# Performance work log

Measured on AMD Instinct MI355X. Metric: run time of the kernel, lower is better.

Reference implementation:

```python
import jax, jax.numpy as jnp
import numpy as np

N_NODES = 110
C = 4096  # in_channels = hidden = out_channels


def setup_inputs() -> dict:
    key = jax.random.key(0)
    ks = jax.random.split(key, 8)
    x = jax.random.normal(ks[0], (N_NODES, C), dtype=jnp.float32)
    adj = jax.random.randint(ks[1], (N_NODES, N_NODES), 0, 2, dtype=jnp.int32)
    # torch.nn.Linear weights stored [out_features, in_features]
    W2 = jax.random.normal(ks[2], (C, C), dtype=jnp.float32) / np.sqrt(C)
    b2 = jax.random.normal(ks[3], (C,), dtype=jnp.float32) * 0.01
    W1 = jax.random.normal(ks[4], (2 * C, C), dtype=jnp.float32) / np.sqrt(2 * C)
    b1 = jax.random.normal(ks[5], (C,), dtype=jnp.float32) * 0.01
    Wl = jax.random.normal(ks[6], (N_NODES, N_NODES), dtype=jnp.float32) / np.sqrt(N_NODES)
    bl = jax.random.normal(ks[7], (N_NODES,), dtype=jnp.float32) * 0.01
    # note: W1 is stored [in=2C, out=C]; W2 [in=C, out=C]; Wl [in=110, out=110]
    return {"x": x, "adj": adj, "W2": W2, "b2": b2, "W1": W1, "b1": b1, "Wl": Wl, "bl": bl}


def reference(x, adj, W2, b2, W1, b1, Wl, bl):
    # FeatGraphConv: h = lin2(x)
    h = x @ W2 + b2  # [N, C]
    # edge_index.nonzero(): adjacency -> edge list (i=src, j=dst); mean-aggregate
    # h[src] at dst. Dense equivalent: column-normalized mask matmul.
    mask = (adj != 0).astype(x.dtype)  # [N, N]
    deg = mask.sum(axis=0)  # in-degree of each target node j
    aggr = (mask.T @ h) / jnp.maximum(deg, 1.0)[:, None]  # [N, C]; 0 for isolated nodes (PyG mean)
    # update: lin1(cat(h, aggr)) then relu (in RegGNN.forward)
    out = jax.nn.relu(jnp.concatenate([h, aggr], axis=1) @ W1 + b1)  # [N, C]
    # x.t(); lin(110,110); x.t()
    out = (out.T @ Wl.T + bl).T  # [N, C]
    return out
```

## Files before the change

### kernel.cpp

```cpp
#include <hip/hip_runtime.h>
#include <hip/hip_fp16.h>

#define C 4096
#define NN 110
#define MPAD 112

typedef _Float16 f16x8 __attribute__((ext_vector_type(8)));
typedef float fx4 __attribute__((ext_vector_type(4)));

__global__ void prep1_kernel(const float* __restrict__ x, _Float16* __restrict__ A1) {
    int idx = blockIdx.x * 256 + threadIdx.x;
    int n = idx >> 12;
    float v = (n < NN) ? x[idx] : 0.f;
    A1[idx] = (_Float16)v;
}

__global__ __launch_bounds__(256, 2)
void mm_kernel(const _Float16* __restrict__ A, const float* __restrict__ B,
               float* __restrict__ Cacc, int lda, int kch) {
    const int t   = threadIdx.x;
    const int wid = blockIdx.x * 4 + (t >> 6);
    const int L   = t & 63;
    const int l15 = L & 15;
    const int q   = L >> 4;
    const int n0  = (wid & 255) * 16;
    const int k0  = (wid >> 8) * kch;

    const _Float16* Ap = A + (size_t)l15 * lda + k0 + q * 8;
    const float*    Bp = B + (size_t)(k0 + q * 8) * C + n0 + l15;

    fx4 acc[7];
    #pragma unroll
    for (int mt = 0; mt < 7; ++mt) acc[mt] = (fx4){0.f, 0.f, 0.f, 0.f};

    float bv0[8], bv1[8];
    f16x8 av0[7], av1[7];

    auto loadB = [&](float (&bv)[8], int kk) {
        #pragma unroll
        for (int j = 0; j < 8; ++j) bv[j] = Bp[(size_t)(kk + j) * C];
    };
    auto loadA = [&](f16x8 (&av)[7], int kk) {
        #pragma unroll
        for (int mt = 0; mt < 7; ++mt)
            av[mt] = *(const f16x8*)(Ap + (size_t)(mt * 16) * lda + kk);
    };
    auto consume = [&](float (&bv)[8], f16x8 (&av)[7]) {
        f16x8 bf;
        #pragma unroll
        for (int j = 0; j < 8; ++j) bf[j] = (_Float16)bv[j];
        #pragma unroll
        for (int mt = 0; mt < 7; ++mt)
            acc[mt] = __builtin_amdgcn_mfma_f32_16x16x32_f16(av[mt], bf, acc[mt], 0, 0, 0);
    };

    loadB(bv0, 0);
    loadA(av0, 0);
    for (int k = 0; k < kch; k += 64) {
        loadB(bv1, k + 32);
        loadA(av1, k + 32);
        consume(bv0, av0);
        if (k + 64 < kch) {
            loadB(bv0, k + 64);
            loadA(av0, k + 64);
        }
        consume(bv1, av1);
    }

    #pragma unroll
    for (int mt = 0; mt < 7; ++mt) {
        #pragma unroll
        for (int r = 0; r < 4; ++r) {
            int row = mt * 16 + q * 4 + r;
            if (row < NN)
                atomicAdd(&Cacc[(size_t)row * C + n0 + l15], acc[mt][r]);
        }
    }
}

__global__ __launch_bounds__(256)
void agg_kernel(const float* __restrict__ h_raw, const int* __restrict__ adj,
                const float* __restrict__ b2, _Float16* __restrict__ A3) {
    __shared__ float hb[NN * 16];
    __shared__ unsigned long long mlo[NN], mhi[NN];
    __shared__ float degs[NN];
    const int t  = threadIdx.x;
    const int c0 = blockIdx.x * 16;

    for (int idx = t; idx < NN * 16; idx += 256) {
        int n = idx >> 4, c = idx & 15;
        float v = h_raw[(size_t)n * C + c0 + c] + b2[c0 + c];
        hb[idx] = v;
        A3[(size_t)n * (2 * C) + c0 + c] = (_Float16)v;
    }
    if (t < 64) {
        int n  = NN + (t >> 5);
        int hs = (t >> 4) & 1;
        int c  = t & 15;
        A3[(size_t)n * (2 * C) + hs * C + c0 + c] = (_Float16)0.f;
    }
    if (t < NN) {
        int j = t;
        unsigned long long lo = 0, hi = 0;
        int dg = 0;
        for (int i = 0; i < 64; ++i) {
            int m = (adj[i * NN + j] != 0);
            lo |= ((unsigned long long)m) << i; dg += m;
        }
        for (int i = 64; i < NN; ++i) {
            int m = (adj[i * NN + j] != 0);
            hi |= ((unsigned long long)m) << (i - 64); dg += m;
        }
        mlo[j] = lo; mhi[j] = hi;
        degs[j] = (float)(dg > 0 ? dg : 1);
    }
    __syncthreads();
    for (int idx = t; idx < NN * 16; idx += 256) {
        int j = idx >> 4, c = idx & 15;
        unsigned long long lo = mlo[j], hi = mhi[j];
        float a = 0.f;
        for (int i = 0; i < 64; ++i)
            if ((lo >> i) & 1) a += hb[i * 16 + c];
        for (int i = 64; i < NN; ++i)
            if ((hi >> (i - 64)) & 1) a += hb[i * 16 + c];
        A3[(size_t)j * (2 * C) + C + c0 + c] = (_Float16)(a / degs[j]);
    }
}

__global__ __launch_bounds__(256)
void fin_kernel(const float* __restrict__ z_raw, const float* __restrict__ b1,
                const float* __restrict__ Wl, const float* __restrict__ bl,
                float* __restrict__ out) {
    __shared__ float zs[NN * 64];
    const int t  = threadIdx.x;
    const int c0 = blockIdx.x * 64;
    const int j  = blockIdx.y * 4 + (t >> 6);
    const int c  = t & 63;

    for (int idx = t; idx < NN * 64; idx += 256) {
        int k = idx >> 6, cc = idx & 63;
        float v = z_raw[(size_t)k * C + c0 + cc] + b1[c0 + cc];
        zs[idx] = fmaxf(v, 0.f);
    }
    __syncthreads();
    if (j < NN) {
        float a = bl[j];
        #pragma unroll 2
        for (int k = 0; k < NN; ++k)
            a += Wl[j * NN + k] * zs[k * 64 + c];
        out[(size_t)j * C + c0 + c] = a;
    }
}

extern "C" void kernel_launch(void* const* d_in, const int* in_sizes, int n_in,
                              void* d_out, int out_size, void* d_ws, size_t ws_size,
                              hipStream_t stream) {
    const float* x   = (const float*)d_in[0];
    const int*   adj = (const int*)d_in[1];
    const float* W2  = (const float*)d_in[2];
    const float* b2  = (const float*)d_in[3];
    const float* W1  = (const float*)d_in[4];
    const float* b1  = (const float*)d_in[5];
    const float* Wl  = (const float*)d_in[6];
    const float* bl  = (const float*)d_in[7];
    float* out = (float*)d_out;

    char* ws = (char*)d_ws;
    float*    h_raw = (float*)(ws);
    float*    z_raw = (float*)(ws + 1802240);
    _Float16* A1    = (_Float16*)(ws + 3604480);
    _Float16* A3    = (_Float16*)(ws + 4521984);

    hipMemsetAsync(d_ws, 0, 3604480, stream);
    prep1_kernel<<<(MPAD * C) / 256, 256, 0, stream>>>(x, A1);
    mm_kernel<<<512, 256, 0, stream>>>(A1, W2, h_raw, C, 512);
    agg_kernel<<<C / 16, 256, 0, stream>>>(h_raw, adj, b2, A3);
    mm_kernel<<<512, 256, 0, stream>>>(A3, W1, z_raw, 2 * C, 1024);
    fin_kernel<<<dim3(C / 64, 28), 256, 0, stream>>>(z_raw, b1, Wl, bl, out);
}
```

Baseline: 391.3 us.

## Stage weight tiles into LDS with async global_load_lds double buffering

```diff
diff --git a/kernel.cpp b/kernel.cpp
--- a/kernel.cpp
+++ b/kernel.cpp
@@ -4,9 +4,15 @@
 #define C 4096
 #define NN 110
 #define MPAD 112
+#define BN 64
+#define BK 128
+#define KCH 512
 
 typedef _Float16 f16x8 __attribute__((ext_vector_type(8)));
 typedef float fx4 __attribute__((ext_vector_type(4)));
+
+#define AS_GLB __attribute__((address_space(1)))
+#define AS_LDS __attribute__((address_space(3)))
 
 __global__ void prep1_kernel(const float* __restrict__ x, _Float16* __restrict__ A1) {
     int idx = blockIdx.x * 256 + threadIdx.x;
@@ -15,56 +21,53 @@
     A1[idx] = (_Float16)v;
 }
 
-__global__ __launch_bounds__(256, 2)
+__global__ __launch_bounds__(256)
 void mm_kernel(const _Float16* __restrict__ A, const float* __restrict__ B,
-               float* __restrict__ Cacc, int lda, int kch) {
+               float* __restrict__ Cacc, int lda) {
+    __shared__ float Bs[2][BK * BN];
     const int t   = threadIdx.x;
-    const int wid = blockIdx.x * 4 + (t >> 6);
+    const int w   = t >> 6;
     const int L   = t & 63;
     const int l15 = L & 15;
     const int q   = L >> 4;
-    const int n0  = (wid & 255) * 16;
-    const int k0  = (wid >> 8) * kch;
+    const int n0  = blockIdx.x * BN;
+    const int k0  = blockIdx.y * KCH;
 
-    const _Float16* Ap = A + (size_t)l15 * lda + k0 + q * 8;
-    const float*    Bp = B + (size_t)(k0 + q * 8) * C + n0 + l15;
+    const float* gsrc = B + (size_t)(k0 + w * 32 + (L >> 4)) * C + n0 + (L & 15) * 4;
+
+    auto stage = [&](int buf, int kc) {
+        #pragma unroll
+        for (int j = 0; j < 8; ++j) {
+            const float* g = gsrc + (size_t)(kc + j * 4) * C;
+            float* l = &Bs[buf][(w * 32 + j * 4) * BN];
+            __builtin_amdgcn_global_load_lds((const AS_GLB void*)g, (AS_LDS void*)l,
+                                             16, 0, 0);
+        }
+    };
 
     fx4 acc[7];
     #pragma unroll
     for (int mt = 0; mt < 7; ++mt) acc[mt] = (fx4){0.f, 0.f, 0.f, 0.f};
 
-    float bv0[8], bv1[8];
-    f16x8 av0[7], av1[7];
-
-    auto loadB = [&](float (&bv)[8], int kk) {
+    stage(0, 0);
+    #pragma unroll 1
+    for (int kc = 0, buf = 0; kc < KCH; kc += BK, buf ^= 1) {
+        __syncthreads();
+        if (kc + BK < KCH) stage(buf ^ 1, kc + BK);
+        const _Float16* Ap = A + (size_t)l15 * lda + k0 + kc + q * 8;
         #pragma unroll
-        for (int j = 0; j < 8; ++j) bv[j] = Bp[(size_t)(kk + j) * C];
-    };
-    auto loadA = [&](f16x8 (&av)[7], int kk) {
-        #pragma unroll
-        for (int mt = 0; mt < 7; ++mt)
-            av[mt] = *(const f16x8*)(Ap + (size_t)(mt * 16) * lda + kk);
-    };
-    auto consume = [&](float (&bv)[8], f16x8 (&av)[7]) {
-        f16x8 bf;
-        #pragma unroll
-        for (int j = 0; j < 8; ++j) bf[j] = (_Float16)bv[j];
-        #pragma unroll
-        for (int mt = 0; mt < 7; ++mt)
-            acc[mt] = __builtin_amdgcn_mfma_f32_16x16x32_f16(av[mt], bf, acc[mt], 0, 0, 0);
-    };
-
-    loadB(bv0, 0);
-    loadA(av0, 0);
-    for (int k = 0; k < kch; k += 64) {
-        loadB(bv1, k + 32);
-        loadA(av1, k + 32);
-        consume(bv0, av0);
-        if (k + 64 < kch) {
-            loadB(bv0, k + 64);
-            loadA(av0, k + 64);
+        for (int s = 0; s < 4; ++s) {
+            f16x8 bfrag;
+            #pragma unroll
+            for (int j = 0; j < 8; ++j)
+                bfrag[j] = (_Float16)Bs[buf][(s * 32 + q * 8 + j) * BN + w * 16 + l15];
+            #pragma unroll
+            for (int mt = 0; mt < 7; ++mt) {
+                f16x8 afrag = *(const f16x8*)(Ap + (size_t)(mt * 16) * lda + s * 32);
+                acc[mt] = __builtin_amdgcn_mfma_f32_16x16x32_f16(afrag, bfrag,
+                                                                 acc[mt], 0, 0, 0);
+            }
         }
-        consume(bv1, av1);
     }
 
     #pragma unroll
@@ -73,7 +76,7 @@
         for (int r = 0; r < 4; ++r) {
             int row = mt * 16 + q * 4 + r;
             if (row < NN)
-                atomicAdd(&Cacc[(size_t)row * C + n0 + l15], acc[mt][r]);
+                atomicAdd(&Cacc[(size_t)row * C + n0 + w * 16 + l15], acc[mt][r]);
         }
     }
 }
@@ -119,10 +122,12 @@
         int j = idx >> 4, c = idx & 15;
         unsigned long long lo = mlo[j], hi = mhi[j];
         float a = 0.f;
+        #pragma unroll 2
         for (int i = 0; i < 64; ++i)
-            if ((lo >> i) & 1) a += hb[i * 16 + c];
+            a = fmaf((float)((lo >> i) & 1ull), hb[i * 16 + c], a);
+        #pragma unroll 2
         for (int i = 64; i < NN; ++i)
-            if ((hi >> (i - 64)) & 1) a += hb[i * 16 + c];
+            a = fmaf((float)((hi >> (i - 64)) & 1ull), hb[i * 16 + c], a);
         A3[(size_t)j * (2 * C) + C + c0 + c] = (_Float16)(a / degs[j]);
     }
 }
@@ -173,8 +178,8 @@
 
     hipMemsetAsync(d_ws, 0, 3604480, stream);
     prep1_kernel<<<(MPAD * C) / 256, 256, 0, stream>>>(x, A1);
-    mm_kernel<<<512, 256, 0, stream>>>(A1, W2, h_raw, C, 512);
+    mm_kernel<<<dim3(C / BN, C / KCH), 256, 0, stream>>>(A1, W2, h_raw, C);
     agg_kernel<<<C / 16, 256, 0, stream>>>(h_raw, adj, b2, A3);
-    mm_kernel<<<512, 256, 0, stream>>>(A3, W1, z_raw, 2 * C, 1024);
+    mm_kernel<<<dim3(C / BN, (2 * C) / KCH), 256, 0, stream>>>(A3, W1, z_raw, 2 * C);
     fin_kernel<<<dim3(C / 64, 28), 256, 0, stream>>>(z_raw, b1, Wl, bl, out);
 }
```

After: 386.2 us. Within noise of the previous version (-1.3%).
